# Kernel tuning notes

Measured on AMD Instinct MI355X. Metric: run time of the kernel, lower is better.

The kernel has to match this reference:

```python
import math
import jax, jax.numpy as jnp
import numpy as np
from jax import lax

SURR_ALPHA = 2.0  # spikingjelly surrogate.ATan default

@jax.custom_vjp
def atan_spike(x):
    # heaviside forward, ATan surrogate backward
    return (x >= 0).astype(x.dtype)

def _atan_fwd(x):
    return atan_spike(x), x

def _atan_bwd(x, g):
    return (g * (SURR_ALPHA / 2) / (1 + (math.pi / 2 * SURR_ALPHA * x) ** 2),)

atan_spike.defvjp(_atan_fwd, _atan_bwd)

def _logit(p):
    return -math.log(1.0 / p - 1.0)

def setup_inputs() -> dict:
    T, B, C = 16, 4096, 1024
    key = jax.random.key(0)
    kx, = jax.random.split(key, 1)
    x = jax.random.normal(kx, (T, B, C), dtype=jnp.float32)
    # parameters initialized exactly as in the torch module
    alpha = jnp.full((C,), _logit((0.6 - 0.5) * 0.5 + 0.5), dtype=jnp.float32)
    beta = jnp.full((C,), _logit((0.8 - 0.5) * 0.5 + 0.5), dtype=jnp.float32)
    gamma = jnp.full((C,), _logit((0.6 - 0.5) * 0.5 + 0.5), dtype=jnp.float32)
    tau = jnp.full((C,), _logit(0.2), dtype=jnp.float32)
    Vth = jnp.full((C,), _logit(0.5), dtype=jnp.float32)
    leak = jnp.full((C,), _logit(0.5 / (T * 2)), dtype=jnp.float32)
    reVth = jnp.full((C,), _logit(0.5), dtype=jnp.float32)
    conduct = jnp.full((T, C), _logit(0.5), dtype=jnp.float32)
    return {"x": x, "tau": tau, "Vth": Vth, "leak": leak, "reVth": reVth,
            "conduct": conduct, "alpha": alpha, "beta": beta, "gamma": gamma}

def reference(x, tau, Vth, leak, reVth, conduct, alpha, beta, gamma):
    dt = x.dtype
    # static_gate=True, soft_mode=False: hard detached gates (al,be,ga all 1 at init)
    al = (alpha > 0).astype(dt)  # [C]
    be = (beta > 0).astype(dt)
    ga = (gamma > 0).astype(dt)
    tau_s = jax.nn.sigmoid(tau)
    Vth_s = jax.nn.sigmoid(Vth)
    leak_s = jax.nn.sigmoid(leak)
    reVth_s = jax.nn.sigmoid(reVth)
    conduct_s = jax.nn.sigmoid(conduct)  # [T, C]

    decay = 1 - al * (1 - tau_s)          # [C]
    leak_term = (1 - al) * leak_s         # [C]

    zeros = jnp.zeros(x.shape[1:], dtype=dt)

    def step(carry, inp):
        u, o = carry
        xt, ct = inp                      # xt: [B,C], ct: [C]
        I_t = xt * (1 - be * (1 - ct))
        u_new = decay * u * (1 - ga * o) - leak_term + I_t - (1 - ga) * reVth_s * o
        o_new = atan_spike(u_new - Vth_s)
        return (u_new, o_new), o_new

    _, out = lax.scan(step, (zeros, zeros), (x, conduct_s))
    return out  # [T, B, C]
```

## Files before the change

kernel.cpp:

```cpp
#include <hip/hip_runtime.h>
#include <math.h>


typedef float f32x4 __attribute__((ext_vector_type(4)));

__device__ __forceinline__ float sigmoidf_acc(float v) {
    return 1.0f / (1.0f + expf(-v));
}

__global__ __launch_bounds__(256) void glif_prep_kernel(
    const float* __restrict__ conduct,
    const float* __restrict__ beta,
    const float* __restrict__ tau,
    const float* __restrict__ Vth,
    const float* __restrict__ leak,
    const float* __restrict__ reVth,
    const float* __restrict__ alpha,
    const float* __restrict__ gamma_,
    float* __restrict__ ws,
    int TC4, int C4)
{
#pragma clang fp contract(off)
    int idx = blockIdx.x * blockDim.x + threadIdx.x;
    if (idx >= TC4) return;
    int c4 = idx & (C4 - 1);

    const f32x4 bev = reinterpret_cast<const f32x4*>(beta)[c4];
    const f32x4 cv  = reinterpret_cast<const f32x4*>(conduct)[idx];
    f32x4 ov;
    #pragma unroll
    for (int j = 0; j < 4; ++j) {
        float be = bev[j] > 0.0f ? 1.0f : 0.0f;
        float ct = sigmoidf_acc(cv[j]);
        ov[j] = 1.0f - be * (1.0f - ct);
    }
    reinterpret_cast<f32x4*>(ws)[idx] = ov;

    if (idx < C4) {
        const int TC = TC4 * 4;
        const f32x4 alv = reinterpret_cast<const f32x4*>(alpha)[c4];
        const f32x4 gav = reinterpret_cast<const f32x4*>(gamma_)[c4];
        const f32x4 tav = reinterpret_cast<const f32x4*>(tau  )[c4];
        const f32x4 vtv = reinterpret_cast<const f32x4*>(Vth  )[c4];
        const f32x4 lkv = reinterpret_cast<const f32x4*>(leak )[c4];
        const f32x4 rvv = reinterpret_cast<const f32x4*>(reVth)[c4];

        f32x4 decay, leakt, vth_s, rvc, ga;
        #pragma unroll
        for (int j = 0; j < 4; ++j) {
            float al = alv[j] > 0.0f ? 1.0f : 0.0f;
            float g  = gav[j] > 0.0f ? 1.0f : 0.0f;
            float tau_s   = sigmoidf_acc(tav[j]);
            float vth_sj  = sigmoidf_acc(vtv[j]);
            float leak_s  = sigmoidf_acc(lkv[j]);
            float reVth_s = sigmoidf_acc(rvv[j]);
            decay[j] = 1.0f - al * (1.0f - tau_s);
            leakt[j] = (1.0f - al) * leak_s;
            vth_s[j] = vth_sj;
            rvc[j]   = (1.0f - g) * reVth_s;
            ga[j]    = g;
        }
        f32x4* p = reinterpret_cast<f32x4*>(ws + TC);
        p[0 * C4 + c4] = decay;
        p[1 * C4 + c4] = leakt;
        p[2 * C4 + c4] = vth_s;
        p[3 * C4 + c4] = rvc;
        p[4 * C4 + c4] = ga;
    }
}

__global__ __launch_bounds__(256) void glif_fwd_kernel(
    const float* __restrict__ x,
    const float* __restrict__ ws,
    float* __restrict__ out,
    int BC4, int C4, int T)
{
#pragma clang fp contract(off)
    int idx = blockIdx.x * blockDim.x + threadIdx.x;
    if (idx >= BC4) return;
    int c4 = idx & (C4 - 1);
    const int TC4 = T * C4;

    const f32x4* __restrict__ p = reinterpret_cast<const f32x4*>(ws) + TC4;
    const f32x4 decay = p[0 * C4 + c4];
    const f32x4 leakt = p[1 * C4 + c4];
    const f32x4 vth_s = p[2 * C4 + c4];
    const f32x4 rvc   = p[3 * C4 + c4];
    const f32x4 ga    = p[4 * C4 + c4];

    float u[4] = {0.0f, 0.0f, 0.0f, 0.0f};
    float o[4] = {0.0f, 0.0f, 0.0f, 0.0f};

    const f32x4* __restrict__ x4  = reinterpret_cast<const f32x4*>(x);
    const f32x4* __restrict__ is4 = reinterpret_cast<const f32x4*>(ws);
    f32x4* __restrict__ o4 = reinterpret_cast<f32x4*>(out);

    const size_t base = (size_t)idx;
    const size_t strd = (size_t)BC4;

    f32x4 xp0 = __builtin_nontemporal_load(&x4[base]);
    f32x4 xp1;
    if (T > 1) xp1 = __builtin_nontemporal_load(&x4[base + strd]);
    f32x4 ivc = is4[c4];

    for (int t = 0; t < T; ++t) {
        f32x4 xp2;
        if (t + 2 < T)
            xp2 = __builtin_nontemporal_load(&x4[base + (size_t)(t + 2) * strd]);
        f32x4 ivn = ivc;
        if (t + 1 < T)
            ivn = is4[(size_t)(t + 1) * (size_t)C4 + (size_t)c4];

        f32x4 ov;
        #pragma unroll
        for (int j = 0; j < 4; ++j) {
            float I  = xp0[j] * ivc[j];
            float un = decay[j] * u[j] * (1.0f - ga[j] * o[j]) - leakt[j] + I
                       - rvc[j] * o[j];
            float on = (un - vth_s[j] >= 0.0f) ? 1.0f : 0.0f;
            u[j] = un;
            o[j] = on;
            ov[j] = on;
        }

        o4[base + (size_t)t * strd] = ov;

        xp0 = xp1;
        xp1 = xp2;
        ivc = ivn;
    }
}

extern "C" void kernel_launch(void* const* d_in, const int* in_sizes, int n_in,
                              void* d_out, int out_size, void* d_ws, size_t ws_size,
                              hipStream_t stream) {
    const float* x       = (const float*)d_in[0];
    const float* tau     = (const float*)d_in[1];
    const float* Vth     = (const float*)d_in[2];
    const float* leak    = (const float*)d_in[3];
    const float* reVth   = (const float*)d_in[4];
    const float* conduct = (const float*)d_in[5];
    const float* alpha   = (const float*)d_in[6];
    const float* beta    = (const float*)d_in[7];
    const float* gamma_  = (const float*)d_in[8];
    float* out = (float*)d_out;

    const int C  = in_sizes[1];
    const int T  = in_sizes[5] / C;
    const long long BC = (long long)in_sizes[0] / T;
    const int BC4 = (int)(BC / 4);
    const int C4  = C / 4;
    const int TC4 = T * C4;

    const int block = 256;

    float* ws = (float*)d_ws;
    glif_prep_kernel<<<(TC4 + block - 1) / block, block, 0, stream>>>(
        conduct, beta, tau, Vth, leak, reVth, alpha, gamma_, ws, TC4, C4);
    glif_fwd_kernel<<<(BC4 + block - 1) / block, block, 0, stream>>>(
        x, ws, out, BC4, C4, T);
}
```

Before: 101.4 us.

## Process two batch halves per thread and specialize kernel for T=16

Each thread now runs two independent recurrences, one in each half of the B*C range, which halves the grid and doubles the loads and stores in flight per thread. A template parameter fixes T=16 at compile time so the time loop can be fully unrolled. The aim is more memory-level parallelism and instruction-level parallelism in a bandwidth-bound scan. The cost is more register pressure and fewer waves, which could lower occupancy. If BC4 is odd, the last element is never processed.

```diff
diff --git a/kernel.cpp b/kernel.cpp
--- a/kernel.cpp
+++ b/kernel.cpp
@@ -69,15 +69,18 @@
     }
 }
 
+template<int TT>
 __global__ __launch_bounds__(256) void glif_fwd_kernel(
     const float* __restrict__ x,
     const float* __restrict__ ws,
     float* __restrict__ out,
-    int BC4, int C4, int T)
+    int BC4, int C4, int Trt)
 {
 #pragma clang fp contract(off)
+    const int T = (TT > 0) ? TT : Trt;
+    const int half = BC4 >> 1;
     int idx = blockIdx.x * blockDim.x + threadIdx.x;
-    if (idx >= BC4) return;
+    if (idx >= half) return;
     int c4 = idx & (C4 - 1);
     const int TC4 = T * C4;
 
@@ -88,45 +91,57 @@
     const f32x4 rvc   = p[3 * C4 + c4];
     const f32x4 ga    = p[4 * C4 + c4];
 
-    float u[4] = {0.0f, 0.0f, 0.0f, 0.0f};
-    float o[4] = {0.0f, 0.0f, 0.0f, 0.0f};
+    float ua[4] = {0.f,0.f,0.f,0.f}, oa[4] = {0.f,0.f,0.f,0.f};
+    float ub[4] = {0.f,0.f,0.f,0.f}, ob[4] = {0.f,0.f,0.f,0.f};
 
     const f32x4* __restrict__ x4  = reinterpret_cast<const f32x4*>(x);
     const f32x4* __restrict__ is4 = reinterpret_cast<const f32x4*>(ws);
     f32x4* __restrict__ o4 = reinterpret_cast<f32x4*>(out);
 
-    const size_t base = (size_t)idx;
-    const size_t strd = (size_t)BC4;
+    const size_t baseA = (size_t)idx;
+    const size_t baseB = (size_t)idx + (size_t)half;
+    const size_t strd  = (size_t)BC4;
 
-    f32x4 xp0 = __builtin_nontemporal_load(&x4[base]);
-    f32x4 xp1;
-    if (T > 1) xp1 = __builtin_nontemporal_load(&x4[base + strd]);
+    f32x4 xa0 = __builtin_nontemporal_load(&x4[baseA]);
+    f32x4 xb0 = __builtin_nontemporal_load(&x4[baseB]);
+    f32x4 xa1, xb1;
+    if (T > 1) {
+        xa1 = __builtin_nontemporal_load(&x4[baseA + strd]);
+        xb1 = __builtin_nontemporal_load(&x4[baseB + strd]);
+    }
     f32x4 ivc = is4[c4];
 
+    #pragma unroll
     for (int t = 0; t < T; ++t) {
-        f32x4 xp2;
-        if (t + 2 < T)
-            xp2 = __builtin_nontemporal_load(&x4[base + (size_t)(t + 2) * strd]);
+        f32x4 xa2, xb2;
+        if (t + 2 < T) {
+            xa2 = __builtin_nontemporal_load(&x4[baseA + (size_t)(t + 2) * strd]);
+            xb2 = __builtin_nontemporal_load(&x4[baseB + (size_t)(t + 2) * strd]);
+        }
         f32x4 ivn = ivc;
         if (t + 1 < T)
             ivn = is4[(size_t)(t + 1) * (size_t)C4 + (size_t)c4];
 
-        f32x4 ov;
+        f32x4 ova, ovb;
         #pragma unroll
         for (int j = 0; j < 4; ++j) {
-            float I  = xp0[j] * ivc[j];
-            float un = decay[j] * u[j] * (1.0f - ga[j] * o[j]) - leakt[j] + I
-                       - rvc[j] * o[j];
-            float on = (un - vth_s[j] >= 0.0f) ? 1.0f : 0.0f;
-            u[j] = un;
-            o[j] = on;
-            ov[j] = on;
+            float Ia  = xa0[j] * ivc[j];
+            float una = decay[j] * ua[j] * (1.0f - ga[j] * oa[j]) - leakt[j] + Ia
+                        - rvc[j] * oa[j];
+            float ona = (una - vth_s[j] >= 0.0f) ? 1.0f : 0.0f;
+            ua[j] = una; oa[j] = ona; ova[j] = ona;
+            float Ib  = xb0[j] * ivc[j];
+            float unb = decay[j] * ub[j] * (1.0f - ga[j] * ob[j]) - leakt[j] + Ib
+                        - rvc[j] * ob[j];
+            float onb = (unb - vth_s[j] >= 0.0f) ? 1.0f : 0.0f;
+            ub[j] = unb; ob[j] = onb; ovb[j] = onb;
         }
 
-        o4[base + (size_t)t * strd] = ov;
+        o4[baseA + (size_t)t * strd] = ova;
+        o4[baseB + (size_t)t * strd] = ovb;
 
-        xp0 = xp1;
-        xp1 = xp2;
+        xa0 = xa1; xa1 = xa2;
+        xb0 = xb1; xb1 = xb2;
         ivc = ivn;
     }
 }
@@ -151,12 +166,19 @@
     const int BC4 = (int)(BC / 4);
     const int C4  = C / 4;
     const int TC4 = T * C4;
+    const int half = BC4 / 2;
 
     const int block = 256;
 
     float* ws = (float*)d_ws;
     glif_prep_kernel<<<(TC4 + block - 1) / block, block, 0, stream>>>(
         conduct, beta, tau, Vth, leak, reVth, alpha, gamma_, ws, TC4, C4);
-    glif_fwd_kernel<<<(BC4 + block - 1) / block, block, 0, stream>>>(
-        x, ws, out, BC4, C4, T);
+
+    if (T == 16) {
+        glif_fwd_kernel<16><<<(half + block - 1) / block, block, 0, stream>>>(
+            x, ws, out, BC4, C4, T);
+    } else {
+        glif_fwd_kernel<0><<<(half + block - 1) / block, block, 0, stream>>>(
+            x, ws, out, BC4, C4, T);
+    }
 }
```

Measured after the change: 106.7 us. +5.2%, slower.
